# Optimization experiments

Hardware: AMD Instinct MI355X
Metric: run time of the kernel (lower is better)

The kernel has to match this reference:

```python
import jax, jax.numpy as jnp
import numpy as np

F_DIM = 256
N_HEADS = 4
D_Q = F_DIM // N_HEADS  # 64
EPS = 1e-6


def layer_norm(x, g, b):
    mu = jnp.mean(x, axis=-1, keepdims=True)
    var = jnp.mean(jnp.square(x - mu), axis=-1, keepdims=True)
    return (x - mu) * jax.lax.rsqrt(var + EPS) * g + b


def linear(x, W, b):
    # torch nn.Linear: y = x @ W.T + b, W: [out, in]
    return jnp.einsum('...i,oi->...o', x, W) + b


def setup_inputs() -> dict:
    key = jax.random.key(0)
    ks = jax.random.split(key, 16)
    f = F_DIM
    inp = {
        'code_map': jax.random.normal(ks[0], (8, 512, f), jnp.float32),
        'texture_map': jax.random.normal(ks[1], (8, 512, f), jnp.float32),
        'Wq': jax.random.normal(ks[2], (N_HEADS * D_Q, f), jnp.float32) * 0.02,
        'bq': jnp.zeros((N_HEADS * D_Q,), jnp.float32),
        'Wk': jax.random.normal(ks[3], (N_HEADS * D_Q, f), jnp.float32) * 0.02,
        'bk': jnp.zeros((N_HEADS * D_Q,), jnp.float32),
        'Wv': jax.random.normal(ks[4], (N_HEADS * D_Q, f), jnp.float32) * 0.02,
        'bv': jnp.zeros((N_HEADS * D_Q,), jnp.float32),
        'Wo': jax.random.normal(ks[5], (f, N_HEADS * D_Q), jnp.float32) * 0.02,
        'bo': jnp.zeros((f,), jnp.float32),
        'ln1_g': jnp.ones((f,), jnp.float32), 'ln1_b': jnp.zeros((f,), jnp.float32),
        'ln2_g': jnp.ones((f,), jnp.float32), 'ln2_b': jnp.zeros((f,), jnp.float32),
        'ffln_g': jnp.ones((f,), jnp.float32), 'ffln_b': jnp.zeros((f,), jnp.float32),
        'W1': jax.random.normal(ks[6], (f, f), jnp.float32) * 0.02,
        'b1': jnp.zeros((f,), jnp.float32),
        'W2': jax.random.normal(ks[7], (f, f), jnp.float32) * 0.02,
        'b2': jnp.zeros((f,), jnp.float32),
    }
    return inp


def reference(code_map, texture_map, Wq, bq, Wk, bk, Wv, bv, Wo, bo,
              ln1_g, ln1_b, ln2_g, ln2_b, ffln_g, ffln_b, W1, b1, W2, b2):
    n_code, V, f = code_map.shape
    bs = texture_map.shape[0]
    h, dq = N_HEADS, D_Q

    # LayerNorms (code side -> ln1, texture side -> ln2); expansion via repeat
    # is a pure broadcast, so keep code side [n_code,...] and texture side [bs,...].
    code2 = layer_norm(code_map, ln1_g, ln1_b)       # [n, V, f]
    tex2 = layer_norm(texture_map, ln2_g, ln2_b)     # [b, V, f]

    q = linear(tex2, Wq, bq).reshape(bs, V, h, dq)    # [b, V, h, d]
    k = linear(code2, Wk, bk).reshape(n_code, V, h, dq)
    v = linear(code2, Wv, bv).reshape(n_code, V, h, dq)

    scale = 1.0 / jnp.sqrt(jnp.asarray(dq, q.dtype))
    # scores: [b, n, h, Vq, Vk]
    scores = jnp.einsum('bqhd,nkhd->bnhqk', q, k) * scale
    attn = jax.nn.softmax(scores, axis=-1)
    ctx = jnp.einsum('bnhqk,nkhd->bnhqd', attn, v)    # [b, n, h, V, d]
    ctx = ctx.transpose(0, 1, 3, 2, 4).reshape(bs, n_code, V, h * dq)
    feat = linear(ctx, Wo, bo)                        # [b, n, V, f]

    x = texture_map[:, None, :, :] + feat             # residual with broadcast
    # ffR: MLP_res_block
    y = layer_norm(x, ffln_g, ffln_b)
    y = linear(jax.nn.relu(linear(y, W1, b1)), W2, b2)
    return x + y
```

## Files before the change

### kernel.cpp

```cpp
#include <hip/hip_runtime.h>
#include <hip/hip_bf16.h>

#define F 256
#define V 512
#define NB 8
#define NC 8
#define NH 4
#define DQ 64
#define EPS 1e-6f
#define CEXPQ 0.18033688f

typedef __hip_bfloat16 bf16;
typedef __attribute__((ext_vector_type(8))) short short8;
typedef __attribute__((ext_vector_type(4))) float f32x4;
typedef __attribute__((ext_vector_type(4))) unsigned uint4v;

__device__ __forceinline__ float b2f(bf16 x){ return __bfloat162float(x); }
__device__ __forceinline__ float shf(short s){
    return __bfloat162float(__builtin_bit_cast(bf16, (unsigned short)s));
}

#define MFMA(a,b,c) __builtin_amdgcn_mfma_f32_16x16x32_bf16((a),(b),(c),0,0,0)

__device__ __forceinline__ unsigned pack2bf(float a, float b){
    unsigned short ua = __builtin_bit_cast(unsigned short, __float2bfloat16(a));
    unsigned short ub = __builtin_bit_cast(unsigned short, __float2bfloat16(b));
    return (unsigned)ua | ((unsigned)ub << 16);
}

__global__ __launch_bounds__(256) void pre_kernel(const float* __restrict__ code,
                          const float* __restrict__ tex,
                          const float* __restrict__ ln1_g, const float* __restrict__ ln1_b,
                          const float* __restrict__ ln2_g, const float* __restrict__ ln2_b,
                          const float* __restrict__ w0, const float* __restrict__ w1,
                          const float* __restrict__ w2, const float* __restrict__ w3,
                          const float* __restrict__ w4, const float* __restrict__ w5,
                          bf16* __restrict__ cn, bf16* __restrict__ tn, bf16* __restrict__ tb,
                          bf16* __restrict__ wdst){
    if (blockIdx.x >= 2048){
        int bid = blockIdx.x - 2048;
        int which = bid >> 6;
        int idx = (((bid & 63) << 8) | threadIdx.x) << 2;
        const float* s = which==0?w0: which==1?w1: which==2?w2: which==3?w3: which==4?w4: w5;
        float4 v = *(const float4*)(s + idx);
        uint2 p; p.x = pack2bf(v.x, v.y); p.y = pack2bf(v.z, v.w);
        *(uint2*)(wdst + which * (F*F) + idx) = p;
        return;
    }
    int w = threadIdx.x >> 6, lane = threadIdx.x & 63;
    int r = blockIdx.x * 4 + w;
    int is_tex = r >> 12;
    int row = r & 4095;
    const float* src = is_tex ? tex : code;
    const float* g   = is_tex ? ln2_g : ln1_g;
    const float* be  = is_tex ? ln2_b : ln1_b;
    bf16* dst        = is_tex ? tn : cn;

    float4 x = *(const float4*)(src + row * F + lane * 4);
    if (is_tex){
        uint2 p; p.x = pack2bf(x.x, x.y); p.y = pack2bf(x.z, x.w);
        *(uint2*)(tb + row * F + lane * 4) = p;
    }
    float s = x.x + x.y + x.z + x.w;
    #pragma unroll
    for(int m = 1; m < 64; m <<= 1) s += __shfl_xor(s, m);
    float mu = s * (1.0f / F);
    float d0 = x.x - mu, d1 = x.y - mu, d2 = x.z - mu, d3 = x.w - mu;
    float q = d0*d0 + d1*d1 + d2*d2 + d3*d3;
    #pragma unroll
    for(int m = 1; m < 64; m <<= 1) q += __shfl_xor(q, m);
    float rs = rsqrtf(q * (1.0f / F) + EPS);
    float4 gg = *(const float4*)(g + lane * 4);
    float4 bb = *(const float4*)(be + lane * 4);
    uint2 p;
    p.x = pack2bf(d0 * rs * gg.x + bb.x, d1 * rs * gg.y + bb.y);
    p.y = pack2bf(d2 * rs * gg.z + bb.z, d3 * rs * gg.w + bb.w);
    *(uint2*)(dst + row * F + lane * 4) = p;
}

__global__ __launch_bounds__(256)
void qkv_kernel(const bf16* __restrict__ cn,
                const bf16* __restrict__ tn,
                const bf16* __restrict__ wbf,
                const float* __restrict__ bq,
                const float* __restrict__ bk,
                const float* __restrict__ bv,
                bf16* __restrict__ qn,
                bf16* __restrict__ k4,
                bf16* __restrict__ v4){
    __shared__ bf16 ts[64][72];
    int which = blockIdx.z;
    const bf16* in   = (which == 0) ? tn : cn;
    const bf16* wb   = wbf + which * (F * F);
    const float* bias = (which == 0) ? bq : (which == 1) ? bk : bv;

    int tid = threadIdx.x;
    int w = tid >> 6, lane = tid & 63;
    int lg = lane >> 4, li = lane & 15;
    int rowbase = blockIdx.x * 64 + w * 16;
    int colbase = blockIdx.y * 64;

    f32x4 acc[4];
    #pragma unroll
    for(int ni = 0; ni < 4; ni++) acc[ni] = (f32x4){0.f,0.f,0.f,0.f};

    const bf16* arow = in + (rowbase + li) * F + lg * 8;
    const bf16* brow = wb + (colbase + li) * F + lg * 8;

    #pragma unroll
    for(int kc = 0; kc < 8; kc++){
        short8 a = *(const short8*)(arow + kc * 32);
        #pragma unroll
        for(int ni = 0; ni < 4; ni++){
            short8 bbf = *(const short8*)(brow + ni * 16 * F + kc * 32);
            acc[ni] = MFMA(a, bbf, acc[ni]);
        }
    }

    float cscale = (which == 0) ? CEXPQ : 1.0f;
    if (which < 2){
        #pragma unroll
        for(int ni = 0; ni < 4; ni++)
            #pragma unroll
            for(int r = 0; r < 4; r++)
                ts[w * 16 + lg * 4 + r][ni * 16 + li] =
                    __float2bfloat16((acc[ni][r] + bias[colbase + ni * 16 + li]) * cscale);
    } else {
        #pragma unroll
        for(int ni = 0; ni < 4; ni++)
            #pragma unroll
            for(int r = 0; r < 4; r++)
                ts[ni * 16 + li][w * 16 + lg * 4 + r] =
                    __float2bfloat16(acc[ni][r] + bias[colbase + ni * 16 + li]);
    }
    __syncthreads();

    if (which == 0){
        int rr = tid >> 2, gg2 = tid & 3;
        *(short8*)(qn + (blockIdx.x * 64 + rr) * F + colbase + gg2 * 16)
            = *(const short8*)&ts[rr][gg2 * 16];
    } else if (which == 1){
        int n = blockIdx.x >> 3;
        int kc2base = (blockIdx.x & 7) * 2;
        int hh = blockIdx.y;
        #pragma unroll
        for(int rep = 0; rep < 2; rep++){
            int c = tid + 256 * rep;
            int f = c >> 6, wf = c & 63;
            int lgp = wf >> 4, lip = wf & 15;
            int kc2l = f >> 2, kt = (f >> 1) & 1, ks = f & 1;
            int keysel = ((lip >> 2) * 8) + kt * 4 + (lip & 3);
            int fi = ((n * 16 + kc2base + kc2l) * 2 + kt) * 8 + hh * 2 + ks;
            *(short8*)(k4 + fi * 512 + lgp * 128 + lip * 8)
                = *(const short8*)&ts[kc2l * 32 + keysel][ks * 32 + lgp * 8];
        }
    } else {
        int col = tid & 63, half = tid >> 6;
        int keybase = blockIdx.x * 64;
        int n = keybase >> 9;
        int keyl = (keybase & (V - 1)) + half * 16;
        int chunk = keyl >> 5, off = keyl & 31;
        *(short8*)(v4 + ((n * 16 + chunk) * F + colbase + col) * 32 + off)
            = *(const short8*)&ts[col][half * 16];
    }
}

__global__ __launch_bounds__(512) void attn_mlp_kernel(const bf16* __restrict__ qn,
                                                       const bf16* __restrict__ k4,
                                                       const bf16* __restrict__ v4,
                                                       const bf16* __restrict__ wbf,
                                                       const float* __restrict__ bo,
                                                       const bf16* __restrict__ tb,
                                                       const float* __restrict__ ffg,
                                                       const float* __restrict__ ffb,
                                                       const float* __restrict__ b1,
                                                       const float* __restrict__ b2,
                                                       float* __restrict__ out){
    __shared__ bf16 xs[64][264];
    int n = blockIdx.x & 7, b = blockIdx.x >> 3, qt = blockIdx.y;
    int tid = threadIdx.x;
    int w = tid >> 6, lane = tid & 63;
    int h = w & 3, qh = w >> 2;
    int lg = lane >> 4, li = lane & 15;

    short8 qB[2][2];
    #pragma unroll
    for(int qq = 0; qq < 2; qq++)
        #pragma unroll
        for(int ks = 0; ks < 2; ks++)
            qB[qq][ks] = *(const short8*)(qn + (b * V + qt * 64 + qh * 32 + qq * 16 + li) * F
                                             + h * DQ + ks * 32 + lg * 8);

    f32x4 o[2][4], ls[2];
    #pragma unroll
    for(int qq = 0; qq < 2; qq++){
        #pragma unroll
        for(int dt = 0; dt < 4; dt++) o[qq][dt] = (f32x4){0.f,0.f,0.f,0.f};
        ls[qq] = (f32x4){0.f,0.f,0.f,0.f};
    }

    short8 ones8;
    #pragma unroll
    for(int j = 0; j < 8; j++) ones8[j] = (short)0x3F80;

    int fel = lg * 128 + li * 8;

    #pragma unroll
    for(int kc = 0; kc < 16; kc++){
        int fb = ((n * 16 + kc) * 2) * 8 + h * 2;
        short8 kA0 = *(const short8*)(k4 + (fb + 0) * 512 + fel);
        short8 kA1 = *(const short8*)(k4 + (fb + 1) * 512 + fel);
        short8 kA2 = *(const short8*)(k4 + (fb + 8) * 512 + fel);
        short8 kA3 = *(const short8*)(k4 + (fb + 9) * 512 + fel);
        const bf16* vb = v4 + ((n * 16 + kc) * F + h * DQ) * 32;
        short8 vA0 = *(const short8*)(vb + (0 * 16 + li) * 32 + lg * 8);
        short8 vA1 = *(const short8*)(vb + (1 * 16 + li) * 32 + lg * 8);
        short8 vA2 = *(const short8*)(vb + (2 * 16 + li) * 32 + lg * 8);
        short8 vA3 = *(const short8*)(vb + (3 * 16 + li) * 32 + lg * 8);

        #pragma unroll
        for(int qq = 0; qq < 2; qq++){
            f32x4 st0 = (f32x4){0.f,0.f,0.f,0.f};
            f32x4 st1 = (f32x4){0.f,0.f,0.f,0.f};
            __builtin_amdgcn_s_setprio(1);
            st0 = MFMA(kA0, qB[qq][0], st0);
            st1 = MFMA(kA2, qB[qq][0], st1);
            st0 = MFMA(kA1, qB[qq][1], st0);
            st1 = MFMA(kA3, qB[qq][1], st1);
            __builtin_amdgcn_s_setprio(0);

            float p0[4], p1[4];
            #pragma unroll
            for(int r = 0; r < 4; r++){
                p0[r] = exp2f(st0[r]);
                p1[r] = exp2f(st1[r]);
            }

            uint4v uv;
            uv.x = pack2bf(p0[0], p0[1]);
            uv.y = pack2bf(p0[2], p0[3]);
            uv.z = pack2bf(p1[0], p1[1]);
            uv.w = pack2bf(p1[2], p1[3]);
            short8 pfrag = __builtin_bit_cast(short8, uv);

            __builtin_amdgcn_s_setprio(1);
            o[qq][0] = MFMA(vA0, pfrag, o[qq][0]);
            o[qq][1] = MFMA(vA1, pfrag, o[qq][1]);
            o[qq][2] = MFMA(vA2, pfrag, o[qq][2]);
            o[qq][3] = MFMA(vA3, pfrag, o[qq][3]);
            ls[qq] = MFMA(ones8, pfrag, ls[qq]);
            __builtin_amdgcn_s_setprio(0);
        }
    }

    float inv[2];
    #pragma unroll
    for(int qq = 0; qq < 2; qq++) inv[qq] = 1.0f / ls[qq][0];

    #pragma unroll
    for(int qq = 0; qq < 2; qq++)
        #pragma unroll
        for(int dt = 0; dt < 4; dt++){
            uint2 pkd;
            pkd.x = pack2bf(o[qq][dt][0] * inv[qq], o[qq][dt][1] * inv[qq]);
            pkd.y = pack2bf(o[qq][dt][2] * inv[qq], o[qq][dt][3] * inv[qq]);
            *(uint2*)&xs[qh * 32 + qq * 16 + li][h * DQ + dt * 16 + lg * 4] = pkd;
        }
    __syncthreads();

    const bf16* Wo = wbf + 3 * (F * F);
    int colbase = w * 32;
    f32x4 xac[4][2];
    #pragma unroll
    for(int mi = 0; mi < 4; mi++)
        #pragma unroll
        for(int ni = 0; ni < 2; ni++) xac[mi][ni] = (f32x4){0.f,0.f,0.f,0.f};
    #pragma unroll
    for(int kc = 0; kc < 8; kc++){
        short8 a[4];
        #pragma unroll
        for(int mi = 0; mi < 4; mi++)
            a[mi] = *(const short8*)&xs[mi * 16 + li][kc * 32 + lg * 8];
        #pragma unroll
        for(int ni = 0; ni < 2; ni++){
            short8 bw = *(const short8*)(Wo + (colbase + ni * 16 + li) * F + kc * 32 + lg * 8);
            #pragma unroll
            for(int mi = 0; mi < 4; mi++)
                xac[mi][ni] = MFMA(a[mi], bw, xac[mi][ni]);
        }
    }
    float xres[4][2][4];
    #pragma unroll
    for(int mi = 0; mi < 4; mi++)
        #pragma unroll
        for(int r = 0; r < 4; r++){
            int qrel = mi * 16 + lg * 4 + r;
            #pragma unroll
            for(int ni = 0; ni < 2; ni++){
                int col = colbase + ni * 16 + li;
                xres[mi][ni][r] = xac[mi][ni][r] + bo[col]
                                + b2f(tb[(b * V + qt * 64 + qrel) * F + col]);
            }
        }
    __syncthreads();
    #pragma unroll
    for(int mi = 0; mi < 4; mi++)
        #pragma unroll
        for(int r = 0; r < 4; r++){
            int qrel = mi * 16 + lg * 4 + r;
            #pragma unroll
            for(int ni = 0; ni < 2; ni++)
                xs[qrel][colbase + ni * 16 + li] = __float2bfloat16(xres[mi][ni][r]);
        }
    __syncthreads();

    int row = tid >> 3, sub = tid & 7;
    short8 xv[4];
    #pragma unroll
    for(int seg = 0; seg < 4; seg++)
        xv[seg] = *(const short8*)&xs[row][sub * 32 + seg * 8];
    float sum = 0.f, sq = 0.f;
    #pragma unroll
    for(int seg = 0; seg < 4; seg++)
        #pragma unroll
        for(int j = 0; j < 8; j++){
            float v0 = shf(xv[seg][j]);
            sum += v0; sq += v0 * v0;
        }
    #pragma unroll
    for(int m = 1; m < 8; m <<= 1){
        sum += __shfl_xor(sum, m);
        sq  += __shfl_xor(sq, m);
    }
    float mu = sum * (1.0f / F);
    float var = sq * (1.0f / F) - mu * mu;
    float rsv = rsqrtf(var + EPS);
    #pragma unroll
    for(int seg = 0; seg < 4; seg++){
        int c = sub * 32 + seg * 8;
        float4 g0 = *(const float4*)(ffg + c);
        float4 g1 = *(const float4*)(ffg + c + 4);
        float4 f0 = *(const float4*)(ffb + c);
        float4 f1 = *(const float4*)(ffb + c + 4);
        float n0 = (shf(xv[seg][0]) - mu) * rsv * g0.x + f0.x;
        float n1 = (shf(xv[seg][1]) - mu) * rsv * g0.y + f0.y;
        float n2 = (shf(xv[seg][2]) - mu) * rsv * g0.z + f0.z;
        float n3 = (shf(xv[seg][3]) - mu) * rsv * g0.w + f0.w;
        float n4 = (shf(xv[seg][4]) - mu) * rsv * g1.x + f1.x;
        float n5 = (shf(xv[seg][5]) - mu) * rsv * g1.y + f1.y;
        float n6 = (shf(xv[seg][6]) - mu) * rsv * g1.z + f1.z;
        float n7 = (shf(xv[seg][7]) - mu) * rsv * g1.w + f1.w;
        uint4v pk;
        pk.x = pack2bf(n0, n1); pk.y = pack2bf(n2, n3);
        pk.z = pack2bf(n4, n5); pk.w = pack2bf(n6, n7);
        *(short8*)&xs[row][c] = __builtin_bit_cast(short8, pk);
    }
    __syncthreads();

    const bf16* W1b = wbf + 4 * (F * F);
    f32x4 hac[4][2];
    #pragma unroll
    for(int mi = 0; mi < 4; mi++)
        #pragma unroll
        for(int ni = 0; ni < 2; ni++) hac[mi][ni] = (f32x4){0.f,0.f,0.f,0.f};
    #pragma unroll
    for(int kc = 0; kc < 8; kc++){
        short8 a[4];
        #pragma unroll
        for(int mi = 0; mi < 4; mi++)
            a[mi] = *(const short8*)&xs[mi * 16 + li][kc * 32 + lg * 8];
        #pragma unroll
        for(int ni = 0; ni < 2; ni++){
            short8 bw = *(const short8*)(W1b + (colbase + ni * 16 + li) * F + kc * 32 + lg * 8);
            #pragma unroll
            for(int mi = 0; mi < 4; mi++)
                hac[mi][ni] = MFMA(a[mi], bw, hac[mi][ni]);
        }
    }
    __syncthreads();
    #pragma unroll
    for(int mi = 0; mi < 4; mi++)
        #pragma unroll
        for(int r = 0; r < 4; r++){
            int rr = mi * 16 + lg * 4 + r;
            #pragma unroll
            for(int ni = 0; ni < 2; ni++){
                int col = colbase + ni * 16 + li;
                xs[rr][col] = __float2bfloat16(fmaxf(hac[mi][ni][r] + b1[col], 0.f));
            }
        }
    __syncthreads();

    const bf16* W2b = wbf + 5 * (F * F);
    f32x4 oac[4][2];
    #pragma unroll
    for(int mi = 0; mi < 4; mi++)
        #pragma unroll
        for(int ni = 0; ni < 2; ni++) oac[mi][ni] = (f32x4){0.f,0.f,0.f,0.f};
    #pragma unroll
    for(int kc = 0; kc < 8; kc++){
        short8 a[4];
        #pragma unroll
        for(int mi = 0; mi < 4; mi++)
            a[mi] = *(const short8*)&xs[mi * 16 + li][kc * 32 + lg * 8];
        #pragma unroll
        for(int ni = 0; ni < 2; ni++){
            short8 bw = *(const short8*)(W2b + (colbase + ni * 16 + li) * F + kc * 32 + lg * 8);
            #pragma unroll
            for(int mi = 0; mi < 4; mi++)
                oac[mi][ni] = MFMA(a[mi], bw, oac[mi][ni]);
        }
    }
    #pragma unroll
    for(int mi = 0; mi < 4; mi++)
        #pragma unroll
        for(int r = 0; r < 4; r++){
            int qrel = mi * 16 + lg * 4 + r;
            int ro = (b * NC + n) * V + qt * 64 + qrel;
            #pragma unroll
            for(int ni = 0; ni < 2; ni++){
                int col = colbase + ni * 16 + li;
                out[ro * F + col] = oac[mi][ni][r] + b2[col] + xres[mi][ni][r];
            }
        }
}

extern "C" void kernel_launch(void* const* d_in, const int* in_sizes, int n_in,
                              void* d_out, int out_size, void* d_ws, size_t ws_size,
                              hipStream_t stream) {
    const float* code_map = (const float*)d_in[0];
    const float* tex_map  = (const float*)d_in[1];
    const float* Wq = (const float*)d_in[2];  const float* bq = (const float*)d_in[3];
    const float* Wk = (const float*)d_in[4];  const float* bk = (const float*)d_in[5];
    const float* Wv = (const float*)d_in[6];  const float* bv = (const float*)d_in[7];
    const float* Wo = (const float*)d_in[8];  const float* bo = (const float*)d_in[9];
    const float* ln1_g = (const float*)d_in[10]; const float* ln1_b = (const float*)d_in[11];
    const float* ln2_g = (const float*)d_in[12]; const float* ln2_b = (const float*)d_in[13];
    const float* ffln_g = (const float*)d_in[14]; const float* ffln_b = (const float*)d_in[15];
    const float* W1 = (const float*)d_in[16]; const float* b1 = (const float*)d_in[17];
    const float* W2 = (const float*)d_in[18]; const float* b2 = (const float*)d_in[19];
    float* out = (float*)d_out;

    bf16* ws  = (bf16*)d_ws;
    bf16* qn  = ws;
    bf16* k4  = qn + 1048576;
    bf16* v4  = k4 + 1048576;
    bf16* cn  = v4 + 1048576;
    bf16* tn  = cn + 1048576;
    bf16* tb  = tn + 1048576;
    bf16* wbf = tb + 1048576;

    pre_kernel<<<2048 + 384, 256, 0, stream>>>(code_map, tex_map, ln1_g, ln1_b, ln2_g, ln2_b,
                                               Wq, Wk, Wv, Wo, W1, W2, cn, tn, tb, wbf);
    qkv_kernel<<<dim3(64, 4, 3), 256, 0, stream>>>(cn, tn, wbf, bq, bk, bv, qn, k4, v4);
    attn_mlp_kernel<<<dim3(64, 8), 512, 0, stream>>>(qn, k4, v4, wbf, bo, tb,
                                                     ffln_g, ffln_b, b1, b2, out);
}
```

Before: 182.7 us.

## Stage K/V chunks in double-buffered LDS via global_load_lds shared across waves

Measured after the change: 193.1 us. +5.7%, slower.

```diff
diff --git a/kernel.cpp b/kernel.cpp
--- a/kernel.cpp
+++ b/kernel.cpp
@@ -21,6 +21,10 @@
 }
 
 #define MFMA(a,b,c) __builtin_amdgcn_mfma_f32_16x16x32_bf16((a),(b),(c),0,0,0)
+
+#define GLL(gsrc, ldst) __builtin_amdgcn_global_load_lds( \
+    (const __attribute__((address_space(1))) unsigned int*)(gsrc), \
+    (__attribute__((address_space(3))) unsigned int*)(ldst), 16, 0, 0)
 
 __device__ __forceinline__ unsigned pack2bf(float a, float b){
     unsigned short ua = __builtin_bit_cast(unsigned short, __float2bfloat16(a));
@@ -176,13 +180,41 @@
                                                        const float* __restrict__ b1,
                                                        const float* __restrict__ b2,
                                                        float* __restrict__ out){
-    __shared__ bf16 xs[64][264];
+    __shared__ __align__(16) char smem[65536];
+    bf16 (*kv)[512] = (bf16(*)[512])smem;
+    bf16 (*xs)[264] = (bf16(*)[264])smem;
+
     int n = blockIdx.x & 7, b = blockIdx.x >> 3, qt = blockIdx.y;
     int tid = threadIdx.x;
     int w = tid >> 6, lane = tid & 63;
     int h = w & 3, qh = w >> 2;
     int lg = lane >> 4, li = lane & 15;
 
+    int h2 = w >> 1;
+    int isV = w & 1;
+    const bf16* ksrc0 = k4 + ((n * 16) * 2 * 8 + h2 * 2) * 512 + lane * 8;
+    const bf16* vsrc0 = v4 + ((n * 16) * F + h2 * DQ) * 32 + li * 32 + lg * 8;
+
+    auto issue_chunk = [&](int kcn){
+        int bsel = kcn & 1;
+        bf16* dst = &kv[(bsel * 4 + h2) * 8 + (isV ? 4 : 0)][0];
+        if (!isV){
+            const bf16* s = ksrc0 + (kcn * 2 * 8) * 512;
+            GLL(s + 0 * 512, dst + 0 * 512);
+            GLL(s + 1 * 512, dst + 1 * 512);
+            GLL(s + 8 * 512, dst + 2 * 512);
+            GLL(s + 9 * 512, dst + 3 * 512);
+        } else {
+            const bf16* s = vsrc0 + (kcn * F) * 32;
+            GLL(s + 0 * 512, dst + 0 * 512);
+            GLL(s + 1 * 512, dst + 1 * 512);
+            GLL(s + 2 * 512, dst + 2 * 512);
+            GLL(s + 3 * 512, dst + 3 * 512);
+        }
+    };
+
+    issue_chunk(0);
+
     short8 qB[2][2];
     #pragma unroll
     for(int qq = 0; qq < 2; qq++)
@@ -203,20 +235,20 @@
     #pragma unroll
     for(int j = 0; j < 8; j++) ones8[j] = (short)0x3F80;
 
-    int fel = lg * 128 + li * 8;
-
     #pragma unroll
     for(int kc = 0; kc < 16; kc++){
-        int fb = ((n * 16 + kc) * 2) * 8 + h * 2;
-        short8 kA0 = *(const short8*)(k4 + (fb + 0) * 512 + fel);
-        short8 kA1 = *(const short8*)(k4 + (fb + 1) * 512 + fel);
-        short8 kA2 = *(const short8*)(k4 + (fb + 8) * 512 + fel);
-        short8 kA3 = *(const short8*)(k4 + (fb + 9) * 512 + fel);
-        const bf16* vb = v4 + ((n * 16 + kc) * F + h * DQ) * 32;
-        short8 vA0 = *(const short8*)(vb + (0 * 16 + li) * 32 + lg * 8);
-        short8 vA1 = *(const short8*)(vb + (1 * 16 + li) * 32 + lg * 8);
-        short8 vA2 = *(const short8*)(vb + (2 * 16 + li) * 32 + lg * 8);
-        short8 vA3 = *(const short8*)(vb + (3 * 16 + li) * 32 + lg * 8);
+        __syncthreads();
+        if (kc < 15) issue_chunk(kc + 1);
+
+        int fbk = ((kc & 1) * 4 + h) * 8;
+        short8 kA0 = *(const short8*)&kv[fbk + 0][lane * 8];
+        short8 kA1 = *(const short8*)&kv[fbk + 1][lane * 8];
+        short8 kA2 = *(const short8*)&kv[fbk + 2][lane * 8];
+        short8 kA3 = *(const short8*)&kv[fbk + 3][lane * 8];
+        short8 vA0 = *(const short8*)&kv[fbk + 4][lane * 8];
+        short8 vA1 = *(const short8*)&kv[fbk + 5][lane * 8];
+        short8 vA2 = *(const short8*)&kv[fbk + 6][lane * 8];
+        short8 vA3 = *(const short8*)&kv[fbk + 7][lane * 8];
 
         #pragma unroll
         for(int qq = 0; qq < 2; qq++){
@@ -256,6 +288,8 @@
     float inv[2];
     #pragma unroll
     for(int qq = 0; qq < 2; qq++) inv[qq] = 1.0f / ls[qq][0];
+
+    __syncthreads();
 
     #pragma unroll
     for(int qq = 0; qq < 2; qq++)
```

## Split attention key range across two wave groups with LDS reduction, 1024-thread blocks

Applied to the files above, without the earlier changes.

New measurement: 381.9 us. 2.09x slower.

```diff
diff --git a/kernel.cpp b/kernel.cpp
--- a/kernel.cpp
+++ b/kernel.cpp
@@ -165,22 +165,25 @@
     }
 }
 
-__global__ __launch_bounds__(512) void attn_mlp_kernel(const bf16* __restrict__ qn,
-                                                       const bf16* __restrict__ k4,
-                                                       const bf16* __restrict__ v4,
-                                                       const bf16* __restrict__ wbf,
-                                                       const float* __restrict__ bo,
-                                                       const bf16* __restrict__ tb,
-                                                       const float* __restrict__ ffg,
-                                                       const float* __restrict__ ffb,
-                                                       const float* __restrict__ b1,
-                                                       const float* __restrict__ b2,
-                                                       float* __restrict__ out){
-    __shared__ bf16 xs[64][264];
+__global__ __launch_bounds__(1024, 8) void attn_mlp_kernel(const bf16* __restrict__ qn,
+                                                           const bf16* __restrict__ k4,
+                                                           const bf16* __restrict__ v4,
+                                                           const bf16* __restrict__ wbf,
+                                                           const float* __restrict__ bo,
+                                                           const bf16* __restrict__ tb,
+                                                           const float* __restrict__ ffg,
+                                                           const float* __restrict__ ffb,
+                                                           const float* __restrict__ b1,
+                                                           const float* __restrict__ b2,
+                                                           float* __restrict__ out){
+    __shared__ __align__(16) char smem[33792 + 18432];
+    bf16 (*xs)[264] = (bf16(*)[264])smem;
+    float (*rb)[64][9] = (float(*)[64][9])(smem + 33792);
+
     int n = blockIdx.x & 7, b = blockIdx.x >> 3, qt = blockIdx.y;
     int tid = threadIdx.x;
     int w = tid >> 6, lane = tid & 63;
-    int h = w & 3, qh = w >> 2;
+    int h = w & 3, qh = (w >> 2) & 1, c = w >> 3;
     int lg = lane >> 4, li = lane & 15;
 
     short8 qB[2][2];
@@ -206,7 +209,8 @@
     int fel = lg * 128 + li * 8;
 
     #pragma unroll
-    for(int kc = 0; kc < 16; kc++){
+    for(int i = 0; i < 8; i++){
+        int kc = c * 8 + i;
         int fb = ((n * 16 + kc) * 2) * 8 + h * 2;
         short8 kA0 = *(const short8*)(k4 + (fb + 0) * 512 + fel);
         short8 kA1 = *(const short8*)(k4 + (fb + 1) * 512 + fel);
@@ -253,54 +257,65 @@
         }
     }
 
-    float inv[2];
-    #pragma unroll
-    for(int qq = 0; qq < 2; qq++) inv[qq] = 1.0f / ls[qq][0];
-
-    #pragma unroll
-    for(int qq = 0; qq < 2; qq++)
-        #pragma unroll
-        for(int dt = 0; dt < 4; dt++){
-            uint2 pkd;
-            pkd.x = pack2bf(o[qq][dt][0] * inv[qq], o[qq][dt][1] * inv[qq]);
-            pkd.y = pack2bf(o[qq][dt][2] * inv[qq], o[qq][dt][3] * inv[qq]);
-            *(uint2*)&xs[qh * 32 + qq * 16 + li][h * DQ + dt * 16 + lg * 4] = pkd;
-        }
-    __syncthreads();
+    {
+        int p = h * 2 + qh;
+        float inv[2] = {0.f, 0.f};
+        #pragma unroll
+        for(int qq = 0; qq < 2; qq++){
+            #pragma unroll
+            for(int half = 0; half < 2; half++){
+                if (c == 1){
+                    #pragma unroll
+                    for(int dd = 0; dd < 2; dd++)
+                        #pragma unroll
+                        for(int r = 0; r < 4; r++)
+                            rb[p][lane][dd * 4 + r] = o[qq][half * 2 + dd][r];
+                    if (half == 0) rb[p][lane][8] = ls[qq][0];
+                }
+                __syncthreads();
+                if (c == 0){
+                    if (half == 0) inv[qq] = 1.0f / (ls[qq][0] + rb[p][lane][8]);
+                    #pragma unroll
+                    for(int dd = 0; dd < 2; dd++){
+                        int dt = half * 2 + dd;
+                        float o0 = (o[qq][dt][0] + rb[p][lane][dd * 4 + 0]) * inv[qq];
+                        float o1 = (o[qq][dt][1] + rb[p][lane][dd * 4 + 1]) * inv[qq];
+                        float o2 = (o[qq][dt][2] + rb[p][lane][dd * 4 + 2]) * inv[qq];
+                        float o3 = (o[qq][dt][3] + rb[p][lane][dd * 4 + 3]) * inv[qq];
+                        uint2 pkd;
+                        pkd.x = pack2bf(o0, o1);
+                        pkd.y = pack2bf(o2, o3);
+                        *(uint2*)&xs[qh * 32 + qq * 16 + li][h * DQ + dt * 16 + lg * 4] = pkd;
+                    }
+                }
+                __syncthreads();
+            }
+        }
+    }
 
     const bf16* Wo = wbf + 3 * (F * F);
-    int colbase = w * 32;
-    f32x4 xac[4][2];
-    #pragma unroll
-    for(int mi = 0; mi < 4; mi++)
-        #pragma unroll
-        for(int ni = 0; ni < 2; ni++) xac[mi][ni] = (f32x4){0.f,0.f,0.f,0.f};
+    int colbase = w * 16;
+    int col = colbase + li;
+    f32x4 xac[4];
+    #pragma unroll
+    for(int mi = 0; mi < 4; mi++) xac[mi] = (f32x4){0.f,0.f,0.f,0.f};
     #pragma unroll
     for(int kc = 0; kc < 8; kc++){
-        short8 a[4];
-        #pragma unroll
-        for(int mi = 0; mi < 4; mi++)
-            a[mi] = *(const short8*)&xs[mi * 16 + li][kc * 32 + lg * 8];
-        #pragma unroll
-        for(int ni = 0; ni < 2; ni++){
-            short8 bw = *(const short8*)(Wo + (colbase + ni * 16 + li) * F + kc * 32 + lg * 8);
-            #pragma unroll
-            for(int mi = 0; mi < 4; mi++)
-                xac[mi][ni] = MFMA(a[mi], bw, xac[mi][ni]);
-        }
-    }
-    float xres[4][2][4];
+        short8 bw = *(const short8*)(Wo + col * F + kc * 32 + lg * 8);
+        #pragma unroll
+        for(int mi = 0; mi < 4; mi++){
+            short8 a = *(const short8*)&xs[mi * 16 + li][kc * 32 + lg * 8];
+            xac[mi] = MFMA(a, bw, xac[mi]);
+        }
+    }
+    float xres[4][4];
     #pragma unroll
     for(int mi = 0; mi < 4; mi++)
         #pragma unroll
         for(int r = 0; r < 4; r++){
             int qrel = mi * 16 + lg * 4 + r;
-            #pragma unroll
-            for(int ni = 0; ni < 2; ni++){
-                int col = colbase + ni * 16 + li;
-                xres[mi][ni][r] = xac[mi][ni][r] + bo[col]
-                                + b2f(tb[(b * V + qt * 64 + qrel) * F + col]);
-            }
+            xres[mi][r] = xac[mi][r] + bo[col]
+                        + b2f(tb[(b * V + qt * 64 + qrel) * F + col]);
         }
     __syncthreads();
     #pragma unroll
@@ -308,73 +323,74 @@
         #pragma unroll
         for(int r = 0; r < 4; r++){
             int qrel = mi * 16 + lg * 4 + r;
-            #pragma unroll
-            for(int ni = 0; ni < 2; ni++)
-                xs[qrel][colbase + ni * 16 + li] = __float2bfloat16(xres[mi][ni][r]);
-        }
-    __syncthreads();
-
-    int row = tid >> 3, sub = tid & 7;
-    short8 xv[4];
-    #pragma unroll
-    for(int seg = 0; seg < 4; seg++)
-        xv[seg] = *(const short8*)&xs[row][sub * 32 + seg * 8];
+            xs[qrel][col] = __float2bfloat16(xres[mi][r]);
+        }
+    __syncthreads();
+
+    int row = tid >> 4, sub = tid & 15;
+    short8 xa = *(const short8*)&xs[row][sub * 16];
+    short8 xb2 = *(const short8*)&xs[row][sub * 16 + 8];
     float sum = 0.f, sq = 0.f;
     #pragma unroll
-    for(int seg = 0; seg < 4; seg++)
-        #pragma unroll
-        for(int j = 0; j < 8; j++){
-            float v0 = shf(xv[seg][j]);
-            sum += v0; sq += v0 * v0;
-        }
-    #pragma unroll
-    for(int m = 1; m < 8; m <<= 1){
+    for(int j = 0; j < 8; j++){
+        float v0 = shf(xa[j]), v1 = shf(xb2[j]);
+        sum += v0 + v1; sq += v0 * v0 + v1 * v1;
+    }
+    #pragma unroll
+    for(int m = 1; m < 16; m <<= 1){
         sum += __shfl_xor(sum, m);
         sq  += __shfl_xor(sq, m);
     }
     float mu = sum * (1.0f / F);
     float var = sq * (1.0f / F) - mu * mu;
     float rsv = rsqrtf(var + EPS);
-    #pragma unroll
-    for(int seg = 0; seg < 4; seg++){
-        int c = sub * 32 + seg * 8;
-        float4 g0 = *(const float4*)(ffg + c);
-        float4 g1 = *(const float4*)(ffg + c + 4);
-        float4 f0 = *(const float4*)(ffb + c);
-        float4 f1 = *(const float4*)(ffb + c + 4);
-        float n0 = (shf(xv[seg][0]) - mu) * rsv * g0.x + f0.x;
-        float n1 = (shf(xv[seg][1]) - mu) * rsv * g0.y + f0.y;
-        float n2 = (shf(xv[seg][2]) - mu) * rsv * g0.z + f0.z;
-        float n3 = (shf(xv[seg][3]) - mu) * rsv * g0.w + f0.w;
-        float n4 = (shf(xv[seg][4]) - mu) * rsv * g1.x + f1.x;
-        float n5 = (shf(xv[seg][5]) - mu) * rsv * g1.y + f1.y;
-        float n6 = (shf(xv[seg][6]) - mu) * rsv * g1.z + f1.z;
-        float n7 = (shf(xv[seg][7]) - mu) * rsv * g1.w + f1.w;
-        uint4v pk;
-        pk.x = pack2bf(n0, n1); pk.y = pack2bf(n2, n3);
-        pk.z = pack2bf(n4, n5); pk.w = pack2bf(n6, n7);
-        *(short8*)&xs[row][c] = __builtin_bit_cast(short8, pk);
+    {
+        int c0 = sub * 16;
+        float4 g0 = *(const float4*)(ffg + c0);
+        float4 g1 = *(const float4*)(ffg + c0 + 4);
+        float4 g2 = *(const float4*)(ffg + c0 + 8);
+        float4 g3 = *(const float4*)(ffg + c0 + 12);
+        float4 f0 = *(const float4*)(ffb + c0);
+        float4 f1 = *(const float4*)(ffb + c0 + 4);
+        float4 f2 = *(const float4*)(ffb + c0 + 8);
+        float4 f3 = *(const float4*)(ffb + c0 + 12);
+        float n0 = (shf(xa[0]) - mu) * rsv * g0.x + f0.x;
+        float n1 = (shf(xa[1]) - mu) * rsv * g0.y + f0.y;
+        float n2 = (shf(xa[2]) - mu) * rsv * g0.z + f0.z;
+        float n3 = (shf(xa[3]) - mu) * rsv * g0.w + f0.w;
+        float n4 = (shf(xa[4]) - mu) * rsv * g1.x + f1.x;
+        float n5 = (shf(xa[5]) - mu) * rsv * g1.y + f1.y;
+        float n6 = (shf(xa[6]) - mu) * rsv * g1.z + f1.z;
+        float n7 = (shf(xa[7]) - mu) * rsv * g1.w + f1.w;
+        float m0 = (shf(xb2[0]) - mu) * rsv * g2.x + f2.x;
+        float m1 = (shf(xb2[1]) - mu) * rsv * g2.y + f2.y;
+        float m2 = (shf(xb2[2]) - mu) * rsv * g2.z + f2.z;
+        float m3 = (shf(xb2[3]) - mu) * rsv * g2.w + f2.w;
+        float m4 = (shf(xb2[4]) - mu) * rsv * g3.x + f3.x;
+        float m5 = (shf(xb2[5]) - mu) * rsv * g3.y + f3.y;
+        float m6 = (shf(xb2[6]) - mu) * rsv * g3.z + f3.z;
+        float m7 = (shf(xb2[7]) - mu) * rsv * g3.w + f3.w;
+        uint4v pa, pb;
+        pa.x = pack2bf(n0, n1); pa.y = pack2bf(n2, n3);
+        pa.z = pack2bf(n4, n5); pa.w = pack2bf(n6, n7);
+        pb.x = pack2bf(m0, m1); pb.y = pack2bf(m2, m3);
+        pb.z = pack2bf(m4, m5); pb.w = pack2bf(m6, m7);
+        *(short8*)&xs[row][sub * 16]     = __builtin_bit_cast(short8, pa);
+        *(short8*)&xs[row][sub * 16 + 8] = __builtin_bit_cast(short8, pb);
     }
     __syncthreads();
 
     const bf16* W1b = wbf + 4 * (F * F);
-    f32x4 hac[4][2];
-    #pragma unroll
-    for(int mi = 0; mi < 4; mi++)
-        #pragma unroll
-        for(int ni = 0; ni < 2; ni++) hac[mi][ni] = (f32x4){0.f,0.f,0.f,0.f};
+    f32x4 hac[4];
+    #pragma unroll
+    for(int mi = 0; mi < 4; mi++) hac[mi] = (f32x4){0.f,0.f,0.f,0.f};
     #pragma unroll
     for(int kc = 0; kc < 8; kc++){
-        short8 a[4];
-        #pragma unroll
-        for(int mi = 0; mi < 4; mi++)
-            a[mi] = *(const short8*)&xs[mi * 16 + li][kc * 32 + lg * 8];
-        #pragma unroll
-        for(int ni = 0; ni < 2; ni++){
-            short8 bw = *(const short8*)(W1b + (colbase + ni * 16 + li) * F + kc * 32 + lg * 8);
-            #pragma unroll
-            for(int mi = 0; mi < 4; mi++)
-                hac[mi][ni] = MFMA(a[mi], bw, hac[mi][ni]);
+        short8 bw = *(const short8*)(W1b + col * F + kc * 32 + lg * 8);
+        #pragma unroll
+        for(int mi = 0; mi < 4; mi++){
+            short8 a = *(const short8*)&xs[mi * 16 + li][kc * 32 + lg * 8];
+            hac[mi] = MFMA(a, bw, hac[mi]);
         }
     }
     __syncthreads();
@@ -383,32 +399,21 @@
         #pragma unroll
         for(int r = 0; r < 4; r++){
             int rr = mi * 16 + lg * 4 + r;
-            #pragma unroll
-            for(int ni = 0; ni < 2; ni++){
-                int col = colbase + ni * 16 + li;
-                xs[rr][col] = __float2bfloat16(fmaxf(hac[mi][ni][r] + b1[col], 0.f));
-            }
+            xs[rr][col] = __float2bfloat16(fmaxf(hac[mi][r] + b1[col], 0.f));
         }
     __syncthreads();
 
     const bf16* W2b = wbf + 5 * (F * F);
-    f32x4 oac[4][2];
-    #pragma unroll
-    for(int mi = 0; mi < 4; mi++)
-        #pragma unroll
-        for(int ni = 0; ni < 2; ni++) oac[mi][ni] = (f32x4){0.f,0.f,0.f,0.f};
+    f32x4 oac[4];
+    #pragma unroll
+    for(int mi = 0; mi < 4; mi++) oac[mi] = (f32x4){0.f,0.f,0.f,0.f};
     #pragma unroll
     for(int kc = 0; kc < 8; kc++){
-        short8 a[4];
-        #pragma unroll
-        for(int mi = 0; mi < 4; mi++)
-            a[mi] = *(const short8*)&xs[mi * 16 + li][kc * 32 + lg * 8];
-        #pragma unroll
-        for(int ni = 0; ni < 2; ni++){
-            short8 bw = *(const short8*)(W2b + (colbase + ni * 16 + li) * F + kc * 32 + lg * 8);
-            #pragma unroll
-            for(int mi = 0; mi < 4; mi++)
-                oac[mi][ni] = MFMA(a[mi], bw, oac[mi][ni]);
+        short8 bw = *(const short8*)(W2b + col * F + kc * 32 + lg * 8);
+        #pragma unroll
+        for(int mi = 0; mi < 4; mi++){
+            short8 a = *(const short8*)&xs[mi * 16 + li][kc * 32 + lg * 8];
+            oac[mi] = MFMA(a, bw, oac[mi]);
         }
     }
     #pragma unroll
@@ -417,11 +422,7 @@
         for(int r = 0; r < 4; r++){
             int qrel = mi * 16 + lg * 4 + r;
             int ro = (b * NC + n) * V + qt * 64 + qrel;
-            #pragma unroll
-            for(int ni = 0; ni < 2; ni++){
-                int col = colbase + ni * 16 + li;
-                out[ro * F + col] = oac[mi][ni][r] + b2[col] + xres[mi][ni][r];
-            }
+            out[ro * F + col] = oac[mi][r] + b2[col] + xres[mi][r];
         }
 }
 
@@ -453,6 +454,6 @@
     pre_kernel<<<2048 + 384, 256, 0, stream>>>(code_map, tex_map, ln1_g, ln1_b, ln2_g, ln2_b,
                                                Wq, Wk, Wv, Wo, W1, W2, cn, tn, tb, wbf);
     qkv_kernel<<<dim3(64, 4, 3), 256, 0, stream>>>(cn, tn, wbf, bq, bk, bv, qn, k4, v4);
-    attn_mlp_kernel<<<dim3(64, 8), 512, 0, stream>>>(qn, k4, v4, wbf, bo, tb,
-                                                     ffln_g, ffln_b, b1, b2, out);
-}
+    attn_mlp_kernel<<<dim3(64, 8), 1024, 0, stream>>>(qn, k4, v4, wbf, bo, tb,
+                                                      ffln_g, ffln_b, b1, b2, out);
+}
```
